# Kernel tuning notes

Hardware: AMD Instinct MI355X
Metric: run time of the kernel (lower is better)

The kernel has to match this reference:

```python
import jax, jax.numpy as jnp
import numpy as np

B, T, D, H = 4, 2048, 1024, 16
HD = D // H  # 64
FF = 4 * D


def layernorm(x, g, b, eps=1e-5):
    mu = jnp.mean(x, axis=-1, keepdims=True)
    var = jnp.mean(jnp.square(x - mu), axis=-1, keepdims=True)
    return (x - mu) * jax.lax.rsqrt(var + eps) * g + b


def setup_inputs() -> dict:
    key = jax.random.key(0)
    ks = jax.random.split(key, 12)
    s_in = 1.0 / np.sqrt(D)
    s_ff = 1.0 / np.sqrt(FF)
    return {
        "x": jax.random.normal(ks[0], (B, T, D), dtype=jnp.float32),
        "mask": jnp.tril(jnp.ones((T, T), dtype=jnp.int32)),  # causal
        "ln1_g": jnp.ones((D,), jnp.float32),
        "ln1_b": jnp.zeros((D,), jnp.float32),
        "Wq": jax.random.uniform(ks[1], (H, D, HD), jnp.float32, -s_in, s_in),
        "bq": jnp.zeros((H, HD), jnp.float32),
        "Wk": jax.random.uniform(ks[2], (H, D, HD), jnp.float32, -s_in, s_in),
        "bk": jnp.zeros((H, HD), jnp.float32),
        "Wv": jax.random.uniform(ks[3], (H, D, HD), jnp.float32, -s_in, s_in),
        "bv": jnp.zeros((H, HD), jnp.float32),
        "Wo": jax.random.uniform(ks[4], (D, D), jnp.float32, -s_in, s_in),
        "bo": jnp.zeros((D,), jnp.float32),
        "ln2_g": jnp.ones((D,), jnp.float32),
        "ln2_b": jnp.zeros((D,), jnp.float32),
        "W1": jax.random.uniform(ks[5], (D, FF), jnp.float32, -s_in, s_in),
        "b1": jnp.zeros((FF,), jnp.float32),
        "W2": jax.random.uniform(ks[6], (FF, D), jnp.float32, -s_ff, s_ff),
        "b2": jnp.zeros((D,), jnp.float32),
    }


def reference(x, mask, ln1_g, ln1_b, Wq, bq, Wk, bk, Wv, bv, Wo, bo,
              ln2_g, ln2_b, W1, b1, W2, b2):
    # --- attention branch (dropout p=0, eval mode) ---
    h = layernorm(x, ln1_g, ln1_b)                      # [B,T,D]
    q = jnp.einsum('btd,hdk->bhtk', h, Wq) + bq[:, None, :]
    k = jnp.einsum('btd,hdk->bhtk', h, Wk) + bk[:, None, :]
    v = jnp.einsum('btd,hdk->bhtk', h, Wv) + bv[:, None, :]
    scores = jnp.einsum('bhqk,bhsk->bhqs', q, k) / jnp.sqrt(jnp.float32(HD))
    scores = jnp.where(mask == 0, -jnp.inf, scores)     # [B,H,T,T]
    attn = jax.nn.softmax(scores, axis=-1)
    ctx = jnp.einsum('bhqs,bhsk->bhqk', attn, v)        # [B,H,T,HD]
    # concat heads along feature dim (head order preserved)
    ctx = jnp.transpose(ctx, (0, 2, 1, 3)).reshape(x.shape[0], x.shape[1], D)
    attn_out = ctx @ Wo + bo
    x = x + attn_out
    # --- GELU FFN branch (torch nn.GELU default = exact erf) ---
    h2 = layernorm(x, ln2_g, ln2_b)
    ff = jax.nn.gelu(h2 @ W1 + b1, approximate=False) @ W2 + b2
    return x + ff
```

## Files before the change

### kernel.cpp

```cpp
#include <hip/hip_runtime.h>
#include <cstdint>
#include <cstddef>

typedef __bf16 bf16x8 __attribute__((ext_vector_type(8)));
typedef float  floatx4 __attribute__((ext_vector_type(4)));

__device__ __forceinline__ uint16_t f2b(float f) {
    uint32_t u = __builtin_bit_cast(uint32_t, f);
    return (uint16_t)((u + 0x7fffu + ((u >> 16) & 1)) >> 16);
}

__device__ __forceinline__ uint16_t bf16bits(float f) {
    __bf16 h = (__bf16)f;
    return __builtin_bit_cast(uint16_t, h);
}

__device__ __forceinline__ void gload_lds16(const void* g, void* l) {
    __builtin_amdgcn_global_load_lds(
        (__attribute__((address_space(1))) void*)(void*)g,
        (__attribute__((address_space(3))) void*)l, 16, 0, 0);
}

template<int CTRL>
__device__ __forceinline__ float dpp_rot(float v) {
    return __builtin_bit_cast(float,
        __builtin_amdgcn_update_dpp(0, __builtin_bit_cast(int, v),
                                    CTRL, 0xf, 0xf, true));
}
__device__ __forceinline__ float rowmax16(float v) {
    v = fmaxf(v, dpp_rot<0x128>(v));
    v = fmaxf(v, dpp_rot<0x124>(v));
    v = fmaxf(v, dpp_rot<0x122>(v));
    v = fmaxf(v, dpp_rot<0x121>(v));
    return v;
}
__device__ __forceinline__ float rowsum16(float v) {
    v += dpp_rot<0x128>(v);
    v += dpp_rot<0x124>(v);
    v += dpp_rot<0x122>(v);
    v += dpp_rot<0x121>(v);
    return v;
}

#define QSCALE 0.18033688011112042f

__global__ __launch_bounds__(256) void repack_qkv(
    const float* __restrict__ Wq, const float* __restrict__ Wk,
    const float* __restrict__ Wv, uint16_t* __restrict__ out)
{
    __shared__ uint16_t tile[32][33];
    const int m = blockIdx.z >> 4, h = blockIdx.z & 15;
    const float* W = (m == 0) ? Wq : (m == 1) ? Wk : Wv;
    const float scl = (m == 0) ? QSCALE : 1.0f;
    const float* src = W + (size_t)h * 1024 * 64;
    const int d0 = blockIdx.x * 32, hd0 = blockIdx.y * 32;
    const int tx = threadIdx.x & 31, ty = threadIdx.x >> 5;
#pragma unroll
    for (int i = 0; i < 4; ++i)
        tile[ty + i * 8][tx] = f2b(src[(size_t)(d0 + ty + i * 8) * 64 + hd0 + tx] * scl);
    __syncthreads();
    uint16_t* dst = out + (size_t)(m * 1024 + h * 64) * 1024;
#pragma unroll
    for (int i = 0; i < 4; ++i)
        dst[(size_t)(hd0 + ty + i * 8) * 1024 + d0 + tx] = tile[tx][ty + i * 8];
}

__global__ __launch_bounds__(256) void transpose_f2b(
    const float* __restrict__ in, uint16_t* __restrict__ out, int R, int C)
{
    __shared__ uint16_t tile[32][33];
    const int c0 = blockIdx.x * 32, r0 = blockIdx.y * 32;
    const int tx = threadIdx.x & 31, ty = threadIdx.x >> 5;
#pragma unroll
    for (int i = 0; i < 4; ++i)
        tile[ty + i * 8][tx] = f2b(in[(size_t)(r0 + ty + i * 8) * C + c0 + tx]);
    __syncthreads();
#pragma unroll
    for (int i = 0; i < 4; ++i)
        out[(size_t)(c0 + ty + i * 8) * R + r0 + tx] = tile[tx][ty + i * 8];
}

__global__ void concat_bias(const float* __restrict__ bq, const float* __restrict__ bk,
                            const float* __restrict__ bv, float* __restrict__ out)
{
    int i = blockIdx.x * 256 + threadIdx.x;
    out[i] = (i < 1024) ? bq[i] * QSCALE : (i < 2048) ? bk[i - 1024] : bv[i - 2048];
}

__global__ __launch_bounds__(256) void transpose_v(
    const uint16_t* __restrict__ qkv, uint16_t* __restrict__ Vt)
{
    __shared__ uint16_t tile[32][33];
    const int bh = blockIdx.z;
    const int b = bh >> 4, h = bh & 15;
    const int t0 = blockIdx.x * 32, hd0 = blockIdx.y * 32;
    const int tx = threadIdx.x & 31, ty = threadIdx.x >> 5;
    const uint16_t* src = qkv + (size_t)b * 2048 * 3072 + 2048 + h * 64;
#pragma unroll
    for (int i = 0; i < 4; ++i)
        tile[ty + i * 8][tx] = src[(size_t)(t0 + ty + i * 8) * 3072 + hd0 + tx];
    __syncthreads();
    uint16_t* dst = Vt + (size_t)bh * 64 * 2048;
#pragma unroll
    for (int i = 0; i < 4; ++i)
        dst[(size_t)(hd0 + ty + i * 8) * 2048 + t0 + tx] = tile[tx][ty + i * 8];
}

__global__ __launch_bounds__(256) void ln_bf16(
    const float* __restrict__ x, const float* __restrict__ g,
    const float* __restrict__ b, uint16_t* __restrict__ out)
{
    const int row = blockIdx.x;
    const int t = threadIdx.x;
    const float4 v = ((const float4*)(x + (size_t)row * 1024))[t];
    float s  = v.x + v.y + v.z + v.w;
    float s2 = v.x * v.x + v.y * v.y + v.z * v.z + v.w * v.w;
#pragma unroll
    for (int o = 32; o > 0; o >>= 1) { s += __shfl_down(s, o); s2 += __shfl_down(s2, o); }
    __shared__ float red[8];
    const int wave = t >> 6, lane = t & 63;
    if (lane == 0) { red[wave] = s; red[4 + wave] = s2; }
    __syncthreads();
    if (t == 0) {
        float a  = red[0] + red[1] + red[2] + red[3];
        float a2 = red[4] + red[5] + red[6] + red[7];
        float mu = a * (1.0f / 1024.0f);
        red[0] = mu;
        red[4] = rsqrtf(a2 * (1.0f / 1024.0f) - mu * mu + 1e-5f);
    }
    __syncthreads();
    const float mu = red[0], rs = red[4];
    const float4 gv = ((const float4*)g)[t];
    const float4 bv = ((const float4*)b)[t];
    ushort4 ov;
    ov.x = f2b((v.x - mu) * rs * gv.x + bv.x);
    ov.y = f2b((v.y - mu) * rs * gv.y + bv.y);
    ov.z = f2b((v.z - mu) * rs * gv.z + bv.z);
    ov.w = f2b((v.w - mu) * rs * gv.w + bv.w);
    ((ushort4*)(out + (size_t)row * 1024))[t] = ov;
}

__global__ __launch_bounds__(256, 3) void gemm_bf16(
    const uint16_t* __restrict__ A, const uint16_t* __restrict__ Bt,
    int M, int N, int K,
    const float* __restrict__ bias, const float* __restrict__ resid,
    float* __restrict__ outF, uint16_t* __restrict__ outB, int mode)
{
    __shared__ __align__(16) uint16_t lds[128 * 128];
    uint16_t* lA = lds;
    uint16_t* lB = lds + 128 * 64;
    const int tid  = threadIdx.x;
    const int wave = tid >> 6, lane = tid & 63;

    const int lid = (int)blockIdx.y * (int)gridDim.x + (int)blockIdx.x;
    const int xcd = lid & 7, t = lid >> 3;
    const int Mb = (M >> 7) >> 3;
    const int perChunk = Mb * 8;
    const int ch = t / perChunk, j = t - ch * perChunk;
    const int m0 = (xcd * Mb + (j & (Mb - 1))) * 128;
    const int n0 = (ch * 8 + (j / Mb)) * 128;

    const int wm = (wave >> 1) * 64, wn = (wave & 1) * 64;
    const int quad = lane >> 4, lrow = lane & 15;
    const int wbase = wave * 64;

    floatx4 acc[4][4] = {};

    const uint16_t* aT = A  + (size_t)m0 * K;
    const uint16_t* bT = Bt + (size_t)n0 * K;

    for (int k0 = 0; k0 < K; k0 += 64) {
        __syncthreads();
#pragma unroll
        for (int i = 0; i < 4; ++i) {
            const int cw = i * 256 + wbase;
            const int q  = cw + lane;
            const int row = q >> 3;
            const int g = ((q & 7) ^ (row & 7)) * 8;
            gload_lds16(aT + (size_t)row * K + k0 + g, &lA[cw * 8]);
            gload_lds16(bT + (size_t)row * K + k0 + g, &lB[cw * 8]);
        }
        __syncthreads();
        bf16x8 af[4][2], bfr[4][2];
#pragma unroll
        for (int mi = 0; mi < 4; ++mi) {
            const int rr = wm + mi * 16 + lrow;
#pragma unroll
            for (int hh = 0; hh < 2; ++hh)
                af[mi][hh] = *(const bf16x8*)
                    &lA[rr * 64 + (((hh * 4 + quad) ^ (rr & 7)) * 8)];
        }
#pragma unroll
        for (int ni = 0; ni < 4; ++ni) {
            const int rr = wn + ni * 16 + lrow;
#pragma unroll
            for (int hh = 0; hh < 2; ++hh)
                bfr[ni][hh] = *(const bf16x8*)
                    &lB[rr * 64 + (((hh * 4 + quad) ^ (rr & 7)) * 8)];
        }
#pragma unroll
        for (int mi = 0; mi < 4; ++mi)
#pragma unroll
            for (int ni = 0; ni < 4; ++ni) {
                acc[mi][ni] = __builtin_amdgcn_mfma_f32_16x16x32_bf16(
                    af[mi][0], bfr[ni][0], acc[mi][ni], 0, 0, 0);
                acc[mi][ni] = __builtin_amdgcn_mfma_f32_16x16x32_bf16(
                    af[mi][1], bfr[ni][1], acc[mi][ni], 0, 0, 0);
            }
    }

    __syncthreads();
    const int r0 = (lane >> 4) * 4;

    if (mode == 1) {
        float* cf = (float*)lds;
#pragma unroll
        for (int p = 0; p < 2; ++p) {
            if ((wave >> 1) == p) {
#pragma unroll
                for (int ni = 0; ni < 4; ++ni) {
                    const int col = wn + ni * 16 + lrow;
                    const float bv = bias[n0 + col];
#pragma unroll
                    for (int mi = 0; mi < 4; ++mi)
#pragma unroll
                        for (int r = 0; r < 4; ++r) {
                            const int row = mi * 16 + r0 + r;
                            const int g = (col >> 2) ^ (((row >> 2) & 1) << 2);
                            cf[row * 128 + g * 4 + (col & 3)] = acc[mi][ni][r] + bv;
                        }
                }
            }
            __syncthreads();
#pragma unroll
            for (int i = 0; i < 8; ++i) {
                const int ci = i * 256 + tid;
                const int row = ci >> 5, cg = ci & 31;
                const int g = cg ^ (((row >> 2) & 1) << 2);
                float4 v = *(const float4*)&cf[row * 128 + g * 4];
                const size_t gidx = (size_t)(m0 + p * 64 + row) * N + n0 + cg * 4;
                const float4 rz = *(const float4*)&resid[gidx];
                v.x += rz.x; v.y += rz.y; v.z += rz.z; v.w += rz.w;
                *(float4*)&outF[gidx] = v;
            }
            __syncthreads();
        }
    } else {
#pragma unroll
        for (int ni = 0; ni < 4; ++ni) {
            const int col = wn + ni * 16 + lrow;
            const float bv = bias[n0 + col];
#pragma unroll
            for (int mi = 0; mi < 4; ++mi)
#pragma unroll
                for (int r = 0; r < 4; ++r) {
                    const int row = wm + mi * 16 + r0 + r;
                    float v = acc[mi][ni][r] + bv;
                    if (mode == 2)
                        v = 0.5f * v * (1.0f + erff(v * 0.70710678118654752f));
                    const int g = (col >> 3) ^ (((row >> 2) & 3) << 1);
                    lds[row * 128 + g * 8 + (col & 7)] = bf16bits(v);
                }
        }
        __syncthreads();
#pragma unroll
        for (int i = 0; i < 8; ++i) {
            const int ci = i * 256 + tid;
            const int row = ci >> 4, cg = ci & 15;
            const int g = cg ^ (((row >> 2) & 3) << 1);
            const bf16x8 v = *(const bf16x8*)&lds[row * 128 + g * 8];
            *(bf16x8*)&outB[(size_t)(m0 + row) * N + n0 + cg * 8] = v;
        }
    }
}

__global__ __launch_bounds__(256, 2) void attn_kernel(
    const uint16_t* __restrict__ qkv, const uint16_t* __restrict__ Vt,
    uint16_t* __restrict__ ctx)
{
    const int h = blockIdx.y, b = blockIdx.z;
    const int tid = threadIdx.x, wave = tid >> 6, lane = tid & 63;
    const int quad = lane >> 4, lcol = lane & 15, lr4 = quad * 4;
    const int sx = lcol & 7;
    const uint16_t* qbase = qkv + (size_t)b * 2048 * 3072;
    const uint16_t* kgb = qbase + 1024 + h * 64;
    const uint16_t* vtb = Vt + (size_t)(b * 16 + h) * 64 * 2048;

    __shared__ __align__(16) uint16_t kbuf[2][64 * 64];
    __shared__ __align__(16) uint16_t vbuf[2][64 * 64];
    __shared__ __align__(16) uint16_t pshm[4][32 * 64];

    const int rr = lane >> 3, sl = lane & 7;
    const int swz = sl ^ rr;

#define STAGE(ktile, bb)                                                        \
    {                                                                           \
        const int _kb = (ktile) * 64;                                           \
        _Pragma("unroll")                                                       \
        for (int i = 0; i < 2; ++i) {                                           \
            const int j = wave * 2 + i;                                         \
            const int r = j * 8 + rr;                                           \
            gload_lds16(kgb + (size_t)(_kb + r) * 3072 + swz * 8,               \
                        &kbuf[bb][j * 512]);                                    \
            gload_lds16(vtb + (size_t)r * 2048 + _kb + swz * 8,                 \
                        &vbuf[bb][j * 512]);                                    \
        }                                                                       \
    }

    for (int pp = 0; pp < 2; ++pp) {
        const int qt = pp ? (int)blockIdx.x : 15 - (int)blockIdx.x;
        const int qr0 = qt * 128 + wave * 32;

        bf16x8 qf[2][2];
#pragma unroll
        for (int mi = 0; mi < 2; ++mi) {
            const uint16_t* qp = qbase + (size_t)(qr0 + mi * 16 + lcol) * 3072 + h * 64;
            qf[mi][0] = *(const bf16x8*)(qp + quad * 8);
            qf[mi][1] = *(const bf16x8*)(qp + 32 + quad * 8);
        }

        floatx4 o[2][4] = {};
        float m_i[2][4], l_i[2][4];
#pragma unroll
        for (int mi = 0; mi < 2; ++mi)
#pragma unroll
            for (int r = 0; r < 4; ++r) { m_i[mi][r] = -1e30f; l_i[mi][r] = 0.f; }

        const int nk = 2 * qt + 2;
        __syncthreads();
        STAGE(0, 0);
        int cur = 0;

        for (int kt = 0; kt < nk; ++kt) {
            const int kb = kt * 64;
            __syncthreads();
            if (kt + 1 < nk) STAGE(kt + 1, cur ^ 1);

            if (kb <= qr0 + 31) {
                bf16x8 kf[4][2];
#pragma unroll
                for (int nt = 0; nt < 4; ++nt) {
                    const int krow = nt * 16 + lcol;
                    kf[nt][0] = *(const bf16x8*)&kbuf[cur][krow * 64 + ((quad ^ sx) * 8)];
                    kf[nt][1] = *(const bf16x8*)&kbuf[cur][krow * 64 + (((quad + 4) ^ sx) * 8)];
                }
#pragma unroll
                for (int mi = 0; mi < 2; ++mi) {
                    floatx4 sv[4];
#pragma unroll
                    for (int nt = 0; nt < 4; ++nt) {
                        floatx4 s = {0.f, 0.f, 0.f, 0.f};
                        s = __builtin_amdgcn_mfma_f32_16x16x32_bf16(qf[mi][0], kf[nt][0], s, 0, 0, 0);
                        s = __builtin_amdgcn_mfma_f32_16x16x32_bf16(qf[mi][1], kf[nt][1], s, 0, 0, 0);
                        sv[nt] = s;
                    }
                    if (kb + 63 > qr0 + mi * 16) {
#pragma unroll
                        for (int nt = 0; nt < 4; ++nt)
#pragma unroll
                            for (int r = 0; r < 4; ++r) {
                                const int row = qr0 + mi * 16 + lr4 + r;
                                const int col = kb + nt * 16 + lcol;
                                if (col > row) sv[nt][r] = -1e30f;
                            }
                    }
#pragma unroll
                    for (int r = 0; r < 4; ++r) {
                        float m = fmaxf(fmaxf(sv[0][r], sv[1][r]),
                                        fmaxf(sv[2][r], sv[3][r]));
                        m = rowmax16(m);
                        const float mn = fmaxf(m_i[mi][r], m);
                        const float alpha = __builtin_amdgcn_exp2f(m_i[mi][r] - mn);
                        m_i[mi][r] = mn;
                        const int row = mi * 16 + lr4 + r;
                        const int rsw = row & 7;
                        float l = 0.f;
#pragma unroll
                        for (int nt = 0; nt < 4; ++nt) {
                            const float p = __builtin_amdgcn_exp2f(sv[nt][r] - mn);
                            l += p;
                            const int col = nt * 16 + lcol;
                            pshm[wave][row * 64 + (((col >> 3) ^ rsw) * 8) + (col & 7)] =
                                bf16bits(p);
                        }
                        l = rowsum16(l);
                        l_i[mi][r] = l_i[mi][r] * alpha + l;
#pragma unroll
                        for (int ht = 0; ht < 4; ++ht) o[mi][ht][r] *= alpha;
                    }
                }
                bf16x8 pf[2][2];
#pragma unroll
                for (int mi = 0; mi < 2; ++mi) {
                    const int prow = mi * 16 + lcol;
                    pf[mi][0] = *(const bf16x8*)&pshm[wave][prow * 64 + ((quad ^ sx) * 8)];
                    pf[mi][1] = *(const bf16x8*)&pshm[wave][prow * 64 + (((quad + 4) ^ sx) * 8)];
                }
#pragma unroll
                for (int ht = 0; ht < 4; ++ht) {
                    const int hd = ht * 16 + lcol;
                    const bf16x8 vf0 = *(const bf16x8*)&vbuf[cur][hd * 64 + ((quad ^ sx) * 8)];
                    const bf16x8 vf1 = *(const bf16x8*)&vbuf[cur][hd * 64 + (((quad + 4) ^ sx) * 8)];
#pragma unroll
                    for (int mi = 0; mi < 2; ++mi) {
                        o[mi][ht] = __builtin_amdgcn_mfma_f32_16x16x32_bf16(pf[mi][0], vf0, o[mi][ht], 0, 0, 0);
                        o[mi][ht] = __builtin_amdgcn_mfma_f32_16x16x32_bf16(pf[mi][1], vf1, o[mi][ht], 0, 0, 0);
                    }
                }
            }
            cur ^= 1;
        }

#pragma unroll
        for (int mi = 0; mi < 2; ++mi)
#pragma unroll
            for (int r = 0; r < 4; ++r) {
                const float inv = 1.0f / l_i[mi][r];
                const int row = qr0 + mi * 16 + lr4 + r;
#pragma unroll
                for (int ht = 0; ht < 4; ++ht)
                    ctx[(size_t)(b * 2048 + row) * 1024 + h * 64 + ht * 16 + lcol] =
                        bf16bits(o[mi][ht][r] * inv);
            }
    }
#undef STAGE
}

extern "C" void kernel_launch(void* const* d_in, const int* in_sizes, int n_in,
                              void* d_out, int out_size, void* d_ws, size_t ws_size,
                              hipStream_t stream)
{
    (void)in_sizes; (void)n_in; (void)out_size; (void)ws_size;
    const float* x     = (const float*)d_in[0];
    const float* ln1_g = (const float*)d_in[2];
    const float* ln1_b = (const float*)d_in[3];
    const float* Wq    = (const float*)d_in[4];
    const float* bq    = (const float*)d_in[5];
    const float* Wk    = (const float*)d_in[6];
    const float* bk    = (const float*)d_in[7];
    const float* Wv    = (const float*)d_in[8];
    const float* bv    = (const float*)d_in[9];
    const float* Wo    = (const float*)d_in[10];
    const float* bo    = (const float*)d_in[11];
    const float* ln2_g = (const float*)d_in[12];
    const float* ln2_b = (const float*)d_in[13];
    const float* W1    = (const float*)d_in[14];
    const float* b1    = (const float*)d_in[15];
    const float* W2    = (const float*)d_in[16];
    const float* b2    = (const float*)d_in[17];
    float* out = (float*)d_out;

    char* w = (char*)d_ws;
    uint16_t* Wqkv_t = (uint16_t*)w;  w += 6291456;
    uint16_t* Wo_t   = (uint16_t*)w;  w += 2097152;
    uint16_t* W1_t   = (uint16_t*)w;  w += 8388608;
    uint16_t* W2_t   = (uint16_t*)w;  w += 8388608;
    float*    bqkv   = (float*)w;     w += 16384;
    float*    x2     = (float*)w;     w += 33554432;
    char* region = w;
    uint16_t* hbuf = (uint16_t*)region;
    uint16_t* qkv  = (uint16_t*)(region + 16777216);
    uint16_t* Vt   = (uint16_t*)(region + 16777216 + 50331648);
    uint16_t* ctx  = hbuf;
    uint16_t* h2   = (uint16_t*)region;
    uint16_t* a1   = (uint16_t*)(region + 16777216);

    repack_qkv<<<dim3(32, 2, 48), 256, 0, stream>>>(Wq, Wk, Wv, Wqkv_t);
    transpose_f2b<<<dim3(32, 32),  256, 0, stream>>>(Wo, Wo_t, 1024, 1024);
    transpose_f2b<<<dim3(128, 32), 256, 0, stream>>>(W1, W1_t, 1024, 4096);
    transpose_f2b<<<dim3(32, 128), 256, 0, stream>>>(W2, W2_t, 4096, 1024);
    concat_bias<<<12, 256, 0, stream>>>(bq, bk, bv, bqkv);
    ln_bf16<<<8192, 256, 0, stream>>>(x, ln1_g, ln1_b, hbuf);
    gemm_bf16<<<dim3(24, 64), 256, 0, stream>>>(hbuf, Wqkv_t, 8192, 3072, 1024,
                                                bqkv, nullptr, nullptr, qkv, 0);
    transpose_v<<<dim3(64, 2, 64), 256, 0, stream>>>(qkv, Vt);
    attn_kernel<<<dim3(8, 16, 4), 256, 0, stream>>>(qkv, Vt, ctx);
    gemm_bf16<<<dim3(8, 64), 256, 0, stream>>>(ctx, Wo_t, 8192, 1024, 1024,
                                               bo, x, x2, nullptr, 1);
    ln_bf16<<<8192, 256, 0, stream>>>(x2, ln2_g, ln2_b, h2);
    gemm_bf16<<<dim3(32, 64), 256, 0, stream>>>(h2, W1_t, 8192, 4096, 1024,
                                                b1, nullptr, nullptr, a1, 2);
    gemm_bf16<<<dim3(8, 64), 256, 0, stream>>>(a1, W2_t, 8192, 1024, 4096,
                                               b2, x2, out, nullptr, 1);
}
```

Measured before the change: 501.6 us.

## Share K/V tiles across paired query tiles and vectorize P stores

The attention kernel now processes both paired query tiles (early and late) in a single pass over key tiles, so each staged K/V tile is loaded once and reused by both instead of being streamed twice. V is stored transposed with a permuted key order so each lane can write its four probabilities as one packed bf16x4 LDS store instead of four scalar stores. This roughly doubles the accumulator and Q-fragment registers per wave, which may raise register pressure under the launch bound of 2 blocks per CU.

Measured after the change: 530.1 us. 5.7% more time.

```diff
diff --git a/kernel.cpp b/kernel.cpp
--- a/kernel.cpp
+++ b/kernel.cpp
@@ -3,6 +3,7 @@
 #include <cstddef>
 
 typedef __bf16 bf16x8 __attribute__((ext_vector_type(8)));
+typedef __bf16 bf16x4 __attribute__((ext_vector_type(4)));
 typedef float  floatx4 __attribute__((ext_vector_type(4)));
 
 __device__ __forceinline__ uint16_t f2b(float f) {
@@ -101,9 +102,11 @@
         tile[ty + i * 8][tx] = src[(size_t)(t0 + ty + i * 8) * 3072 + hd0 + tx];
     __syncthreads();
     uint16_t* dst = Vt + (size_t)bh * 64 * 2048;
+    const int key = t0 + tx;
+    const int kp  = (key & ~63) | (((key & 15) << 2) | ((key >> 4) & 3));
 #pragma unroll
     for (int i = 0; i < 4; ++i)
-        dst[(size_t)(hd0 + ty + i * 8) * 2048 + t0 + tx] = tile[tx][ty + i * 8];
+        dst[(size_t)(hd0 + ty + i * 8) * 2048 + kp] = tile[tx][ty + i * 8];
 }
 
 __global__ __launch_bounds__(256) void ln_bf16(
@@ -289,6 +292,7 @@
     __shared__ __align__(16) uint16_t kbuf[2][64 * 64];
     __shared__ __align__(16) uint16_t vbuf[2][64 * 64];
     __shared__ __align__(16) uint16_t pshm[4][32 * 64];
+    uint16_t* psw = &pshm[wave][0];
 
     const int rr = lane >> 3, sl = lane & 7;
     const int swz = sl ^ rr;
@@ -307,123 +311,139 @@
         }                                                                       \
     }
 
-    for (int pp = 0; pp < 2; ++pp) {
-        const int qt = pp ? (int)blockIdx.x : 15 - (int)blockIdx.x;
-        const int qr0 = qt * 128 + wave * 32;
-
-        bf16x8 qf[2][2];
-#pragma unroll
-        for (int mi = 0; mi < 2; ++mi) {
-            const uint16_t* qp = qbase + (size_t)(qr0 + mi * 16 + lcol) * 3072 + h * 64;
-            qf[mi][0] = *(const bf16x8*)(qp + quad * 8);
-            qf[mi][1] = *(const bf16x8*)(qp + 32 + quad * 8);
-        }
-
-        floatx4 o[2][4] = {};
-        float m_i[2][4], l_i[2][4];
-#pragma unroll
-        for (int mi = 0; mi < 2; ++mi)
-#pragma unroll
-            for (int r = 0; r < 4; ++r) { m_i[mi][r] = -1e30f; l_i[mi][r] = 0.f; }
-
-        const int nk = 2 * qt + 2;
+    const int qtA = 15 - (int)blockIdx.x, qtB = (int)blockIdx.x;
+    const int qr0A = qtA * 128 + wave * 32;
+    const int qr0B = qtB * 128 + wave * 32;
+
+    bf16x8 qfA[2][2], qfB[2][2];
+#pragma unroll
+    for (int mi = 0; mi < 2; ++mi) {
+        const uint16_t* qpA = qbase + (size_t)(qr0A + mi * 16 + lcol) * 3072 + h * 64;
+        qfA[mi][0] = *(const bf16x8*)(qpA + quad * 8);
+        qfA[mi][1] = *(const bf16x8*)(qpA + 32 + quad * 8);
+        const uint16_t* qpB = qbase + (size_t)(qr0B + mi * 16 + lcol) * 3072 + h * 64;
+        qfB[mi][0] = *(const bf16x8*)(qpB + quad * 8);
+        qfB[mi][1] = *(const bf16x8*)(qpB + 32 + quad * 8);
+    }
+
+    floatx4 oA[2][4] = {}, oB[2][4] = {};
+    float mA[2][4], lA_[2][4], mB[2][4], lB_[2][4];
+#pragma unroll
+    for (int mi = 0; mi < 2; ++mi)
+#pragma unroll
+        for (int r = 0; r < 4; ++r) {
+            mA[mi][r] = -1e30f; lA_[mi][r] = 0.f;
+            mB[mi][r] = -1e30f; lB_[mi][r] = 0.f;
+        }
+
+    const int nk = 2 * qtA + 2;
+    STAGE(0, 0);
+    int cur = 0;
+
+    for (int kt = 0; kt < nk; ++kt) {
+        const int kb = kt * 64;
         __syncthreads();
-        STAGE(0, 0);
-        int cur = 0;
-
-        for (int kt = 0; kt < nk; ++kt) {
-            const int kb = kt * 64;
-            __syncthreads();
-            if (kt + 1 < nk) STAGE(kt + 1, cur ^ 1);
-
-            if (kb <= qr0 + 31) {
-                bf16x8 kf[4][2];
+        if (kt + 1 < nk) STAGE(kt + 1, cur ^ 1);
+
+        bf16x8 kf[4][2];
+#pragma unroll
+        for (int nt = 0; nt < 4; ++nt) {
+            const int krow = nt * 16 + lcol;
+            kf[nt][0] = *(const bf16x8*)&kbuf[cur][krow * 64 + ((quad ^ sx) * 8)];
+            kf[nt][1] = *(const bf16x8*)&kbuf[cur][krow * 64 + (((quad + 4) ^ sx) * 8)];
+        }
+
+        auto process = [&](const bf16x8 (&qf)[2][2], floatx4 (&o)[2][4],
+                           float (&m_i)[2][4], float (&l_i)[2][4], const int qr0) {
+#pragma unroll
+            for (int mi = 0; mi < 2; ++mi) {
+                floatx4 sv[4];
 #pragma unroll
                 for (int nt = 0; nt < 4; ++nt) {
-                    const int krow = nt * 16 + lcol;
-                    kf[nt][0] = *(const bf16x8*)&kbuf[cur][krow * 64 + ((quad ^ sx) * 8)];
-                    kf[nt][1] = *(const bf16x8*)&kbuf[cur][krow * 64 + (((quad + 4) ^ sx) * 8)];
+                    floatx4 s = {0.f, 0.f, 0.f, 0.f};
+                    s = __builtin_amdgcn_mfma_f32_16x16x32_bf16(qf[mi][0], kf[nt][0], s, 0, 0, 0);
+                    s = __builtin_amdgcn_mfma_f32_16x16x32_bf16(qf[mi][1], kf[nt][1], s, 0, 0, 0);
+                    sv[nt] = s;
                 }
+                if (kb + 63 > qr0 + mi * 16) {
+#pragma unroll
+                    for (int nt = 0; nt < 4; ++nt)
+#pragma unroll
+                        for (int r = 0; r < 4; ++r) {
+                            const int row = qr0 + mi * 16 + lr4 + r;
+                            const int col = kb + nt * 16 + lcol;
+                            if (col > row) sv[nt][r] = -1e30f;
+                        }
+                }
+                floatx4 alphav;
+#pragma unroll
+                for (int r = 0; r < 4; ++r) {
+                    float m = fmaxf(fmaxf(sv[0][r], sv[1][r]),
+                                    fmaxf(sv[2][r], sv[3][r]));
+                    m = rowmax16(m);
+                    const float mn = fmaxf(m_i[mi][r], m);
+                    const float alpha = __builtin_amdgcn_exp2f(m_i[mi][r] - mn);
+                    m_i[mi][r] = mn;
+                    const float p0 = __builtin_amdgcn_exp2f(sv[0][r] - mn);
+                    const float p1 = __builtin_amdgcn_exp2f(sv[1][r] - mn);
+                    const float p2 = __builtin_amdgcn_exp2f(sv[2][r] - mn);
+                    const float p3 = __builtin_amdgcn_exp2f(sv[3][r] - mn);
+                    float l = p0 + p1 + p2 + p3;
+                    l = rowsum16(l);
+                    l_i[mi][r] = l_i[mi][r] * alpha + l;
+                    alphav[r] = alpha;
+                    const int row = mi * 16 + lr4 + r;
+                    bf16x4 pk4;
+                    pk4[0] = (__bf16)p0; pk4[1] = (__bf16)p1;
+                    pk4[2] = (__bf16)p2; pk4[3] = (__bf16)p3;
+                    const int chunk = (lcol >> 1) ^ (row & 7);
+                    *(bf16x4*)&psw[row * 64 + chunk * 8 + (lcol & 1) * 4] = pk4;
+                }
+#pragma unroll
+                for (int ht = 0; ht < 4; ++ht) o[mi][ht] *= alphav;
+            }
+            bf16x8 pf[2][2];
+#pragma unroll
+            for (int mi = 0; mi < 2; ++mi) {
+                const int prow = mi * 16 + lcol;
+                pf[mi][0] = *(const bf16x8*)&psw[prow * 64 + ((quad ^ sx) * 8)];
+                pf[mi][1] = *(const bf16x8*)&psw[prow * 64 + (((quad + 4) ^ sx) * 8)];
+            }
+#pragma unroll
+            for (int ht = 0; ht < 4; ++ht) {
+                const int hd = ht * 16 + lcol;
+                const bf16x8 vf0 = *(const bf16x8*)&vbuf[cur][hd * 64 + ((quad ^ sx) * 8)];
+                const bf16x8 vf1 = *(const bf16x8*)&vbuf[cur][hd * 64 + (((quad + 4) ^ sx) * 8)];
 #pragma unroll
                 for (int mi = 0; mi < 2; ++mi) {
-                    floatx4 sv[4];
-#pragma unroll
-                    for (int nt = 0; nt < 4; ++nt) {
-                        floatx4 s = {0.f, 0.f, 0.f, 0.f};
-                        s = __builtin_amdgcn_mfma_f32_16x16x32_bf16(qf[mi][0], kf[nt][0], s, 0, 0, 0);
-                        s = __builtin_amdgcn_mfma_f32_16x16x32_bf16(qf[mi][1], kf[nt][1], s, 0, 0, 0);
-                        sv[nt] = s;
-                    }
-                    if (kb + 63 > qr0 + mi * 16) {
-#pragma unroll
-                        for (int nt = 0; nt < 4; ++nt)
-#pragma unroll
-                            for (int r = 0; r < 4; ++r) {
-                                const int row = qr0 + mi * 16 + lr4 + r;
-                                const int col = kb + nt * 16 + lcol;
-                                if (col > row) sv[nt][r] = -1e30f;
-                            }
-                    }
-#pragma unroll
-                    for (int r = 0; r < 4; ++r) {
-                        float m = fmaxf(fmaxf(sv[0][r], sv[1][r]),
-                                        fmaxf(sv[2][r], sv[3][r]));
-                        m = rowmax16(m);
-                        const float mn = fmaxf(m_i[mi][r], m);
-                        const float alpha = __builtin_amdgcn_exp2f(m_i[mi][r] - mn);
-                        m_i[mi][r] = mn;
-                        const int row = mi * 16 + lr4 + r;
-                        const int rsw = row & 7;
-                        float l = 0.f;
-#pragma unroll
-                        for (int nt = 0; nt < 4; ++nt) {
-                            const float p = __builtin_amdgcn_exp2f(sv[nt][r] - mn);
-                            l += p;
-                            const int col = nt * 16 + lcol;
-                            pshm[wave][row * 64 + (((col >> 3) ^ rsw) * 8) + (col & 7)] =
-                                bf16bits(p);
-                        }
-                        l = rowsum16(l);
-                        l_i[mi][r] = l_i[mi][r] * alpha + l;
-#pragma unroll
-                        for (int ht = 0; ht < 4; ++ht) o[mi][ht][r] *= alpha;
-                    }
+                    o[mi][ht] = __builtin_amdgcn_mfma_f32_16x16x32_bf16(pf[mi][0], vf0, o[mi][ht], 0, 0, 0);
+                    o[mi][ht] = __builtin_amdgcn_mfma_f32_16x16x32_bf16(pf[mi][1], vf1, o[mi][ht], 0, 0, 0);
                 }
-                bf16x8 pf[2][2];
-#pragma unroll
-                for (int mi = 0; mi < 2; ++mi) {
-                    const int prow = mi * 16 + lcol;
-                    pf[mi][0] = *(const bf16x8*)&pshm[wave][prow * 64 + ((quad ^ sx) * 8)];
-                    pf[mi][1] = *(const bf16x8*)&pshm[wave][prow * 64 + (((quad + 4) ^ sx) * 8)];
-                }
-#pragma unroll
-                for (int ht = 0; ht < 4; ++ht) {
-                    const int hd = ht * 16 + lcol;
-                    const bf16x8 vf0 = *(const bf16x8*)&vbuf[cur][hd * 64 + ((quad ^ sx) * 8)];
-                    const bf16x8 vf1 = *(const bf16x8*)&vbuf[cur][hd * 64 + (((quad + 4) ^ sx) * 8)];
-#pragma unroll
-                    for (int mi = 0; mi < 2; ++mi) {
-                        o[mi][ht] = __builtin_amdgcn_mfma_f32_16x16x32_bf16(pf[mi][0], vf0, o[mi][ht], 0, 0, 0);
-                        o[mi][ht] = __builtin_amdgcn_mfma_f32_16x16x32_bf16(pf[mi][1], vf1, o[mi][ht], 0, 0, 0);
-                    }
-                }
-            }
-            cur ^= 1;
-        }
-
-#pragma unroll
-        for (int mi = 0; mi < 2; ++mi)
-#pragma unroll
-            for (int r = 0; r < 4; ++r) {
-                const float inv = 1.0f / l_i[mi][r];
-                const int row = qr0 + mi * 16 + lr4 + r;
-#pragma unroll
-                for (int ht = 0; ht < 4; ++ht)
-                    ctx[(size_t)(b * 2048 + row) * 1024 + h * 64 + ht * 16 + lcol] =
-                        bf16bits(o[mi][ht][r] * inv);
-            }
+            }
+        };
+
+        if (kb <= qr0A + 31) process(qfA, oA, mA, lA_, qr0A);
+        if (kb <= qr0B + 31) process(qfB, oB, mB, lB_, qr0B);
+        cur ^= 1;
     }
 #undef STAGE
+
+#pragma unroll
+    for (int mi = 0; mi < 2; ++mi)
+#pragma unroll
+        for (int r = 0; r < 4; ++r) {
+            const float invA = 1.0f / lA_[mi][r];
+            const float invB = 1.0f / lB_[mi][r];
+            const int rowA = qr0A + mi * 16 + lr4 + r;
+            const int rowB = qr0B + mi * 16 + lr4 + r;
+#pragma unroll
+            for (int ht = 0; ht < 4; ++ht) {
+                ctx[(size_t)(b * 2048 + rowA) * 1024 + h * 64 + ht * 16 + lcol] =
+                    bf16bits(oA[mi][ht][r] * invA);
+                ctx[(size_t)(b * 2048 + rowB) * 1024 + h * 64 + ht * 16 + lcol] =
+                    bf16bits(oB[mi][ht][r] * invB);
+            }
+        }
 }
 
 extern "C" void kernel_launch(void* const* d_in, const int* in_sizes, int n_in,
```
